# Kernel tuning notes

Hardware: AMD Instinct MI355X
Metric: run time of the kernel (lower is better)

The kernel has to match this reference:

```python
import jax, jax.numpy as jnp
import numpy as np

N_HEADS = 16
D_MODEL = 1024
SEQ = 1024
WIDTH = 32
BATCH = 4


def _make_graph(n, w, seed=0):
    # Mirrors sparse_attention_graph: normal offsets around each node index,
    # mod n, then per-row duplicates are replaced by global-ish tokens 0,1,...
    rng = np.random.default_rng(seed)
    pulls = rng.normal(0.0, float(w), size=(n, w)).astype(np.int64)
    adj = (pulls + np.arange(n)[:, None]) % n
    rows = []
    for r in adj:
        u = np.unique(r)
        i = 0
        while u.shape[0] < w:
            d = w - u.shape[0]
            u = np.unique(np.concatenate([np.arange(i, i + d), u]))
            i += d
        rows.append(np.sort(u))
    return jnp.asarray(np.stack(rows), dtype=jnp.int32)


def setup_inputs() -> dict:
    key = jax.random.key(0)
    ks = jax.random.split(key, 5)
    scale = 1.0 / np.sqrt(D_MODEL).astype(np.float32)
    return {
        "hidden_states": jax.random.normal(ks[0], (BATCH, SEQ, D_MODEL), jnp.float32),
        "wq_kernel": jax.random.normal(ks[1], (D_MODEL, D_MODEL), jnp.float32) * scale,
        "wq_bias": jnp.zeros((D_MODEL,), jnp.float32),
        "wk_kernel": jax.random.normal(ks[2], (D_MODEL, D_MODEL), jnp.float32) * scale,
        "wk_bias": jnp.zeros((D_MODEL,), jnp.float32),
        "wv_kernel": jax.random.normal(ks[3], (D_MODEL, D_MODEL), jnp.float32) * scale,
        "wv_bias": jnp.zeros((D_MODEL,), jnp.float32),
        "wo_kernel": jax.random.normal(ks[4], (D_MODEL, D_MODEL), jnp.float32) * scale,
        "wo_bias": jnp.zeros((D_MODEL,), jnp.float32),
        "graph": _make_graph(SEQ, WIDTH),
    }


def reference(hidden_states, wq_kernel, wq_bias, wk_kernel, wk_bias,
              wv_kernel, wv_bias, wo_kernel, wo_bias, graph):
    B, N, D = hidden_states.shape
    H = N_HEADS
    depth = D // H

    def split_heads(x):
        return x.reshape(B, N, H, depth).transpose(0, 2, 1, 3)  # [B,H,N,depth]

    q = split_heads(hidden_states @ wq_kernel + wq_bias)
    k = split_heads(hidden_states @ wk_kernel + wk_bias)
    v = split_heads(hidden_states @ wv_kernel + wv_bias)

    # Gather neighbor keys per node: [B,H,N,W,depth]; dot only on graph edges.
    kg = k[:, :, graph, :]
    dots = jnp.einsum('bhnd,bhnwd->bhnw', q, kg)

    # Scatter edge dots into dense [B,H,N,N] score matrix; non-edges stay 0,
    # exactly as dot_circle_product does (softmax then runs over the FULL row).
    rows = jnp.arange(N)[:, None]  # broadcasts with graph [N,W]
    scores = jnp.zeros((B, H, N, N), hidden_states.dtype).at[:, :, rows, graph].set(dots)

    attn = jax.nn.softmax(scores / jnp.sqrt(jnp.asarray(depth, scores.dtype)), axis=-1)
    out = jnp.einsum('bhij,bhjd->bhid', attn, v)          # [B,H,N,depth]
    out = out.transpose(0, 2, 1, 3).reshape(B, N, D)      # merge heads
    output = out @ wo_kernel + wo_bias
    return (output, attn)
```

## Files before the change

kernel.cpp:

```cpp
#include <hip/hip_runtime.h>
#include <hip/hip_bf16.h>

constexpr int B = 4;
constexpr int N = 1024;
constexpr int D = 1024;
constexpr int H = 16;
constexpr int DEPTH = 64;
constexpr int W = 32;
constexpr int LDQKV = 3072;
constexpr int SROWS = 8704;

typedef _Float16 f16x8 __attribute__((ext_vector_type(8)));
typedef float f32x4 __attribute__((ext_vector_type(4)));
typedef unsigned short us8 __attribute__((ext_vector_type(8)));
typedef unsigned short us4 __attribute__((ext_vector_type(4)));

__device__ __forceinline__ float h2f(unsigned short u) {
  return (float)__builtin_bit_cast(_Float16, u);
}

__device__ __forceinline__ void load_lds16(const void* g, void* l) {
  unsigned int lo = (unsigned int)(unsigned long long)l;
  __builtin_amdgcn_global_load_lds(
      (const __attribute__((address_space(1))) unsigned int*)g,
      (__attribute__((address_space(3))) unsigned int*)lo, 16, 0, 0);
}

__device__ __forceinline__ void fill_row(float* rowf, const float* pbuf,
                                         const float* basebuf,
                                         const int* graph, float* attn,
                                         int row, int t) {
  const int n = row & (N - 1);
  const float base = basebuf[row];
  f32x4* rw = (f32x4*)rowf;
  rw[t] = (f32x4){base, base, base, base};
  __syncthreads();
  if (t < W) rowf[graph[n * W + t]] = pbuf[(size_t)row * W + t];
  __syncthreads();
  __builtin_nontemporal_store(rw[t], (f32x4*)(attn + (size_t)row * N) + t);
}

__global__ __launch_bounds__(256) void prep_all(
    const float* __restrict__ hidden, const float* __restrict__ wq,
    const float* __restrict__ wk, const float* __restrict__ wv,
    const float* __restrict__ wo, const float* __restrict__ bq,
    const float* __restrict__ bk, const float* __restrict__ bv,
    unsigned short* __restrict__ A16, unsigned short* __restrict__ BTh,
    unsigned short* __restrict__ WoTh, float* __restrict__ biasq) {
  __shared__ float sf[64][65];
  const int t = threadIdx.x;
  int blk = blockIdx.x;

  if (blk < 2048) {
    const size_t i = ((size_t)blk * 256 + t) * 8;
    float4 a = *(const float4*)(hidden + i);
    float4 b = *(const float4*)(hidden + i + 4);
    float xs[8] = {a.x, a.y, a.z, a.w, b.x, b.y, b.z, b.w};
    us8 hv;
#pragma unroll
    for (int j = 0; j < 8; j++)
      hv[j] = __builtin_bit_cast(unsigned short, (_Float16)xs[j]);
    *(us8*)(A16 + i) = hv;
    return;
  }
  blk -= 2048;
  if (blk < 1024) {
    const int which = blk >> 8;
    const int sub = blk & 255;
    const float* w = which == 0 ? wq : which == 1 ? wk : which == 2 ? wv : wo;
    unsigned short* oh = which < 3 ? BTh : WoTh;
    const int rowOff = which < 3 ? which * 1024 : 0;

    const int tn = (sub & 15) * 64;
    const int tk = (sub >> 4) * 64;
#pragma unroll
    for (int i = 0; i < 4; i++) {
      int f = i * 256 + t;
      int r = f >> 4, c4 = (f & 15) * 4;
      float4 v = *(const float4*)(w + (size_t)(tk + r) * 1024 + tn + c4);
      sf[r][c4 + 0] = v.x; sf[r][c4 + 1] = v.y;
      sf[r][c4 + 2] = v.z; sf[r][c4 + 3] = v.w;
    }
    __syncthreads();
    const int n = t >> 2;
    const int kc = (t & 3) * 16;
    us8 hv[2];
#pragma unroll
    for (int half = 0; half < 2; half++) {
#pragma unroll
      for (int j = 0; j < 8; j++) {
        float x = sf[kc + half * 8 + j][n];
        hv[half][j] = __builtin_bit_cast(unsigned short, (_Float16)x);
      }
    }
    size_t dst = (size_t)(rowOff + tn + n) * 1024 + tk + kc;
    *(us8*)(oh + dst) = hv[0];
    *(us8*)(oh + dst + 8) = hv[1];
    return;
  }
  blk -= 1024;
  int i = blk * 256 + t;
  biasq[i] = i < 1024 ? bq[i] : (i < 2048 ? bk[i - 1024] : bv[i - 2048]);
}

__global__ __launch_bounds__(256, 2) void gemm_qkv(
    const unsigned short* __restrict__ A16, const unsigned short* __restrict__ BTh,
    const float* __restrict__ bias, unsigned short* __restrict__ Cout,
    float* __restrict__ vpart, int K, int Nn) {
  __shared__ __align__(16) unsigned short sA[2 * 128 * 32];
  __shared__ __align__(16) unsigned short sB[2 * 256 * 32];
  __shared__ float vred[2][2][8][16];

  const int tid = threadIdx.x;
  const int lane = tid & 63;
  const int wave = tid >> 6;
  const int wr = wave >> 1, wc = wave & 1;

  const int gx = gridDim.x;
  const int nwg = gx * gridDim.y;
  int bid = blockIdx.y * gx + blockIdx.x;
  bid = (bid & 7) * (nwg >> 3) + (bid >> 3);
  const int bm = (bid / gx) * 128;
  const int bn = (bid % gx) * 256;

  size_t aoff[2];
  int ldsA[2];
#pragma unroll
  for (int c = 0; c < 2; c++) {
    const int chunk = wave + 4 * c;
    const int e = chunk * 512 + lane * 8;
    const int r = e >> 5;
    const int kpos = (e >> 3) & 3;
    const int ksrc = kpos ^ ((r >> 1) & 3);
    aoff[c] = (size_t)(bm + r) * K + ksrc * 8;
    ldsA[c] = chunk * 512;
  }
  size_t boff[4];
  int ldsB[4];
#pragma unroll
  for (int c = 0; c < 4; c++) {
    const int chunk = wave + 4 * c;
    const int e = chunk * 512 + lane * 8;
    const int r = e >> 5;
    const int kpos = (e >> 3) & 3;
    const int ksrc = kpos ^ ((r >> 1) & 3);
    boff[c] = (size_t)(bn + r) * K + ksrc * 8;
    ldsB[c] = chunk * 512;
  }

  const int fr = lane & 15;
  const int fkg = lane >> 4;

  int aroff[4], broff[8];
#pragma unroll
  for (int m = 0; m < 4; m++) {
    const int ra = wr * 64 + m * 16 + fr;
    aroff[m] = ra * 32 + ((fkg ^ ((ra >> 1) & 3)) << 3);
  }
#pragma unroll
  for (int n = 0; n < 8; n++) {
    const int rb = wc * 128 + n * 16 + fr;
    broff[n] = rb * 32 + ((fkg ^ ((rb >> 1) & 3)) << 3);
  }

  f32x4 acc[4][8] = {};

  const int NT = K >> 5;
#pragma unroll
  for (int c = 0; c < 2; c++) load_lds16(A16 + aoff[c], sA + ldsA[c]);
#pragma unroll
  for (int c = 0; c < 4; c++) load_lds16(BTh + boff[c], sB + ldsB[c]);
  __syncthreads();

  int cur = 0;
  for (int t = 0; t < NT; t++) {
    const int boA = cur * (128 * 32);
    const int boB = cur * (256 * 32);
    const int nxA = (cur ^ 1) * (128 * 32);
    const int nxB = (cur ^ 1) * (256 * 32);
    if (t + 1 < NT) {
      const int k0 = (t + 1) << 5;
#pragma unroll
      for (int c = 0; c < 2; c++) load_lds16(A16 + aoff[c] + k0, sA + nxA + ldsA[c]);
#pragma unroll
      for (int c = 0; c < 4; c++) load_lds16(BTh + boff[c] + k0, sB + nxB + ldsB[c]);
    }
    f16x8 a[4], bh[8];
#pragma unroll
    for (int m = 0; m < 4; m++) a[m] = *(const f16x8*)(sA + boA + aroff[m]);
#pragma unroll
    for (int n = 0; n < 8; n++) bh[n] = *(const f16x8*)(sB + boB + broff[n]);
    __builtin_amdgcn_s_setprio(1);
#pragma unroll
    for (int m = 0; m < 4; m++)
#pragma unroll
      for (int n = 0; n < 8; n++)
        acc[m][n] = __builtin_amdgcn_mfma_f32_16x16x32_f16(a[m], bh[n], acc[m][n], 0, 0, 0);
    __builtin_amdgcn_s_setprio(0);
    __syncthreads();
    cur ^= 1;
  }

#pragma unroll
  for (int m = 0; m < 4; m++) {
    const int row = bm + wr * 64 + m * 16 + fkg * 4;
#pragma unroll
    for (int n = 0; n < 8; n++) {
      const int col = bn + wc * 128 + n * 16 + fr;
      const float bsv = bias[col];
#pragma unroll
      for (int j = 0; j < 4; j++) {
        const float v = acc[m][n][j] + bsv;
        Cout[(size_t)(row + j) * Nn + col] =
            __builtin_bit_cast(unsigned short, (_Float16)v);
      }
    }
  }

  if (bn >= 2048) {
    float csum[8];
#pragma unroll
    for (int n = 0; n < 8; n++) {
      float s = 0.f;
#pragma unroll
      for (int m = 0; m < 4; m++)
#pragma unroll
        for (int j = 0; j < 4; j++) s += acc[m][n][j];
      s += __shfl_xor(s, 16);
      s += __shfl_xor(s, 32);
      csum[n] = s;
    }
    if (fkg == 0) {
#pragma unroll
      for (int n = 0; n < 8; n++) vred[wr][wc][n][fr] = csum[n];
    }
    __syncthreads();
    if (wr == 0 && fkg == 0) {
#pragma unroll
      for (int n = 0; n < 8; n++) {
        const int d = bn - 2048 + wc * 128 + n * 16 + fr;
        vpart[(size_t)(bm >> 7) * 1024 + d] = csum[n] + vred[1][wc][n][fr];
      }
    }
  }
}

__global__ __launch_bounds__(256) void vsum_comb(const float* __restrict__ vpart,
                                                 const float* __restrict__ biasq,
                                                 float* __restrict__ vsum) {
  const int i = blockIdx.x * 256 + threadIdx.x;
  const int b = i >> 10, d = i & 1023;
  float s = 1024.0f * biasq[2048 + d];
#pragma unroll
  for (int c = 0; c < 8; c++) s += vpart[(size_t)(b * 8 + c) * 1024 + d];
  vsum[i] = s;
}

__global__ __launch_bounds__(256) void attn_pass1(
    const unsigned short* __restrict__ qkv16, const float* __restrict__ vsum,
    const int* __restrict__ graph, float* __restrict__ pbuf,
    float* __restrict__ basebuf, unsigned short* __restrict__ O16,
    float* __restrict__ attn) {
  const int blk = blockIdx.x;
  const int n = blk & (N - 1);
  const int hg = (blk >> 10) & 3;
  const int b = blk >> 12;
  const int wave = threadIdx.x >> 6;
  const int lane = threadIdx.x & 63;
  const int h = hg * 4 + wave;
  const int bid = (b * H + h) * N + n;

  __shared__ float q_sh[4][DEPTH];
  __shared__ int g_sh[W];
  __shared__ float p_sh[4][W];
  __shared__ float rowbuf[4][N];

  const unsigned short* qrow = qkv16 + (size_t)(b * N + n) * LDQKV + h * DEPTH;
  q_sh[wave][lane] = h2f(qrow[lane]);
  if (threadIdx.x < W) g_sh[threadIdx.x] = graph[n * W + threadIdx.x];
  __syncthreads();

  const int w = lane >> 1;
  const int half = lane & 1;
  const unsigned short* krow =
      qkv16 + 1024 + (size_t)(b * N + g_sh[w]) * LDQKV + h * DEPTH + half * 32;
  float acc = 0.f;
#pragma unroll
  for (int j8 = 0; j8 < 4; j8++) {
    us8 kv = *(const us8*)(krow + j8 * 8);
    const float* qh = &q_sh[wave][half * 32 + j8 * 8];
#pragma unroll
    for (int e = 0; e < 8; e++) acc += h2f(kv[e]) * qh[e];
  }
  acc += __shfl_xor(acc, 1);
  const float dot = acc * 0.125f;

  float m = dot;
#pragma unroll
  for (int off = 2; off < 64; off <<= 1) m = fmaxf(m, __shfl_xor(m, off));
  m = fmaxf(m, 0.f);

  const float e = expf(dot - m);
  float s = e;
#pragma unroll
  for (int off = 1; off < 64; off <<= 1) s += __shfl_xor(s, off);
  s *= 0.5f;

  const float em = expf(-m);
  const float Z = (float)(N - W) * em + s;
  const float inv = 1.f / Z;
  const float base = em * inv;
  const float pw = e * inv;

  if (half == 0) p_sh[wave][w] = pw;
  __syncthreads();

  const bool fused = (bid >= SROWS);
  if (!fused) {
    if (half == 0) pbuf[(size_t)bid * W + w] = pw;
    if (lane == 0) basebuf[bid] = base;
  }

  const unsigned short* vbase = qkv16 + 2048;
  const int col = h * DEPTH + lane;
  float ov = base * vsum[b * D + col];
#pragma unroll 4
  for (int ww = 0; ww < W; ww++) {
    ov += (p_sh[wave][ww] - base) *
          h2f(vbase[(size_t)(b * N + g_sh[ww]) * LDQKV + col]);
  }
  _Float16 hh = (_Float16)ov;
  O16[(size_t)(b * N + n) * D + col] = __builtin_bit_cast(unsigned short, hh);

  f32x4* rw = (f32x4*)rowbuf[wave];
  f32x4 b4v = {base, base, base, base};
#pragma unroll
  for (int i = 0; i < 4; i++) rw[lane + 64 * i] = b4v;
  __syncthreads();
  if (fused && half == 0) rowbuf[wave][g_sh[w]] = pw;
  __syncthreads();
  if (fused) {
    f32x4* dst = (f32x4*)(attn + (size_t)bid * N);
#pragma unroll
    for (int i = 0; i < 4; i++)
      __builtin_nontemporal_store(rw[lane + 64 * i], dst + lane + 64 * i);
  }
}

__global__ __launch_bounds__(256, 4) void gemm_o_fill(
    const unsigned short* __restrict__ A16, const unsigned short* __restrict__ BTh,
    const float* __restrict__ bias, float* __restrict__ Cout,
    const float* __restrict__ pbuf, const float* __restrict__ basebuf,
    const int* __restrict__ graph, float* __restrict__ attn, int K, int Nn) {
  __shared__ __align__(16) unsigned short sA[2 * 128 * 32];
  __shared__ __align__(16) unsigned short sB[2 * 128 * 32];

  const int blk = blockIdx.x;
  if (blk >= 256) {
    fill_row((float*)sA, pbuf, basebuf, graph, attn, blk - 256, threadIdx.x);
    return;
  }

  const int tid = threadIdx.x;
  const int lane = tid & 63;
  const int wave = tid >> 6;
  const int wr = wave >> 1, wc = wave & 1;

  int bid = blk;
  bid = (bid & 7) * 32 + (bid >> 3);
  const int bm = (bid >> 3) * 128;
  const int bn = (bid & 7) * 128;

  size_t aoff[2], boff[2];
  int ldsoff[2];
#pragma unroll
  for (int c = 0; c < 2; c++) {
    const int chunk = wave + 4 * c;
    const int e = chunk * 512 + lane * 8;
    const int r = e >> 5;
    const int kpos = (e >> 3) & 3;
    const int ksrc = kpos ^ ((r >> 1) & 3);
    aoff[c] = (size_t)(bm + r) * K + ksrc * 8;
    boff[c] = (size_t)(bn + r) * K + ksrc * 8;
    ldsoff[c] = chunk * 512;
  }

  const int fr = lane & 15;
  const int fkg = lane >> 4;

  int aroff[4], broff[4];
#pragma unroll
  for (int m = 0; m < 4; m++) {
    const int ra = wr * 64 + m * 16 + fr;
    aroff[m] = ra * 32 + ((fkg ^ ((ra >> 1) & 3)) << 3);
    const int rb = wc * 64 + m * 16 + fr;
    broff[m] = rb * 32 + ((fkg ^ ((rb >> 1) & 3)) << 3);
  }

  f32x4 acc[4][4] = {};

  const int NT = K >> 5;
#pragma unroll
  for (int c = 0; c < 2; c++) {
    load_lds16(A16 + aoff[c], sA + ldsoff[c]);
    load_lds16(BTh + boff[c], sB + ldsoff[c]);
  }
  __syncthreads();

  int cur = 0;
  for (int t = 0; t < NT; t++) {
    const int bo_ = cur * (128 * 32);
    const int nx_ = (cur ^ 1) * (128 * 32);
    if (t + 1 < NT) {
      const int k0 = (t + 1) << 5;
#pragma unroll
      for (int c = 0; c < 2; c++) {
        load_lds16(A16 + aoff[c] + k0, sA + nx_ + ldsoff[c]);
        load_lds16(BTh + boff[c] + k0, sB + nx_ + ldsoff[c]);
      }
    }
    f16x8 a[4], bh[4];
#pragma unroll
    for (int m = 0; m < 4; m++) a[m] = *(const f16x8*)(sA + bo_ + aroff[m]);
#pragma unroll
    for (int n = 0; n < 4; n++) bh[n] = *(const f16x8*)(sB + bo_ + broff[n]);
    __builtin_amdgcn_s_setprio(1);
#pragma unroll
    for (int m = 0; m < 4; m++)
#pragma unroll
      for (int n = 0; n < 4; n++)
        acc[m][n] = __builtin_amdgcn_mfma_f32_16x16x32_f16(a[m], bh[n], acc[m][n], 0, 0, 0);
    __builtin_amdgcn_s_setprio(0);
    __syncthreads();
    cur ^= 1;
  }

#pragma unroll
  for (int m = 0; m < 4; m++) {
    const int row = bm + wr * 64 + m * 16 + fkg * 4;
#pragma unroll
    for (int n = 0; n < 4; n++) {
      const int col = bn + wc * 64 + n * 16 + fr;
      const float bsv = bias[col];
#pragma unroll
      for (int j = 0; j < 4; j++)
        Cout[(size_t)(row + j) * Nn + col] = acc[m][n][j] + bsv;
    }
  }
}

__global__ __launch_bounds__(256) void attn_fill_last(
    const float* __restrict__ pbuf, const float* __restrict__ basebuf,
    const int* __restrict__ graph, float* __restrict__ attn) {
  __shared__ __align__(16) float rowf[N];
  fill_row(rowf, pbuf, basebuf, graph, attn, 6144 + blockIdx.x, threadIdx.x);
}

extern "C" void kernel_launch(void* const* d_in, const int* in_sizes, int n_in,
                              void* d_out, int out_size, void* d_ws, size_t ws_size,
                              hipStream_t stream) {
  const float* hidden = (const float*)d_in[0];
  const float* wq = (const float*)d_in[1];
  const float* bq = (const float*)d_in[2];
  const float* wk = (const float*)d_in[3];
  const float* bk = (const float*)d_in[4];
  const float* wv = (const float*)d_in[5];
  const float* bv = (const float*)d_in[6];
  const float* wo = (const float*)d_in[7];
  const float* bo = (const float*)d_in[8];
  const int* graph = (const int*)d_in[9];

  float* out0 = (float*)d_out;
  float* attnp = out0 + (size_t)B * N * D;

  const size_t M1 = (size_t)1024 * 1024;
  unsigned short* qkv16 = (unsigned short*)attnp;
  unsigned short* A16 = (unsigned short*)(attnp + 6 * M1);
  unsigned short* O16 = A16;
  unsigned short* WoTh = (unsigned short*)(attnp + 8 * M1);
  unsigned short* BTh = (unsigned short*)(attnp + 8 * M1 + 524288);

  float* pbuf = (float*)d_ws;
  float* basebuf = pbuf + (size_t)B * H * N * W;
  float* vsumb = basebuf + (size_t)B * H * N;
  float* biasq = pbuf;
  float* vpart = pbuf + 4096;

  prep_all<<<3084, 256, 0, stream>>>(hidden, wq, wk, wv, wo, bq, bk, bv,
                                     A16, BTh, WoTh, biasq);

  gemm_qkv<<<dim3(12, 32), 256, 0, stream>>>(A16, BTh, biasq, qkv16, vpart,
                                             1024, 3072);

  vsum_comb<<<16, 256, 0, stream>>>(vpart, biasq, vsumb);

  attn_pass1<<<B * 4 * N, 256, 0, stream>>>(qkv16, vsumb, graph, pbuf, basebuf,
                                            O16, attnp);

  gemm_o_fill<<<256 + 6144, 256, 0, stream>>>(O16, WoTh, bo, out0, pbuf,
                                              basebuf, graph, attnp,
                                              1024, 1024);

  attn_fill_last<<<8704 - 6144, 256, 0, stream>>>(pbuf, basebuf, graph, attnp);
}
```

Measured before the change: 146.2 us.

## Fuse hidden-state fp16 conversion into QKV GEMM and drop vsum kernel

The QKV GEMM now loads fp32 hidden states straight into LDS with a new swizzle and converts them to fp16 on the fly. This removes the separate conversion pass in prep_all and its A16 buffer round trip. The vsum_comb kernel is also removed, and each attn_pass1 thread now sums the 8 V-column partials itself, which drops one launch but repeats that small reduction in every block. The cost is twice the LDS traffic for A and extra conversion instructions inside the GEMM main loop. The reduction scratch space now reuses sA after a barrier.

New measurement: 148.3 us. About the same (+1.5%).

```diff
diff --git a/kernel.cpp b/kernel.cpp
--- a/kernel.cpp
+++ b/kernel.cpp
@@ -41,29 +41,15 @@
 }
 
 __global__ __launch_bounds__(256) void prep_all(
-    const float* __restrict__ hidden, const float* __restrict__ wq,
-    const float* __restrict__ wk, const float* __restrict__ wv,
-    const float* __restrict__ wo, const float* __restrict__ bq,
-    const float* __restrict__ bk, const float* __restrict__ bv,
-    unsigned short* __restrict__ A16, unsigned short* __restrict__ BTh,
+    const float* __restrict__ wq, const float* __restrict__ wk,
+    const float* __restrict__ wv, const float* __restrict__ wo,
+    const float* __restrict__ bq, const float* __restrict__ bk,
+    const float* __restrict__ bv, unsigned short* __restrict__ BTh,
     unsigned short* __restrict__ WoTh, float* __restrict__ biasq) {
   __shared__ float sf[64][65];
   const int t = threadIdx.x;
   int blk = blockIdx.x;
 
-  if (blk < 2048) {
-    const size_t i = ((size_t)blk * 256 + t) * 8;
-    float4 a = *(const float4*)(hidden + i);
-    float4 b = *(const float4*)(hidden + i + 4);
-    float xs[8] = {a.x, a.y, a.z, a.w, b.x, b.y, b.z, b.w};
-    us8 hv;
-#pragma unroll
-    for (int j = 0; j < 8; j++)
-      hv[j] = __builtin_bit_cast(unsigned short, (_Float16)xs[j]);
-    *(us8*)(A16 + i) = hv;
-    return;
-  }
-  blk -= 2048;
   if (blk < 1024) {
     const int which = blk >> 8;
     const int sub = blk & 255;
@@ -104,12 +90,11 @@
 }
 
 __global__ __launch_bounds__(256, 2) void gemm_qkv(
-    const unsigned short* __restrict__ A16, const unsigned short* __restrict__ BTh,
+    const float* __restrict__ hidden, const unsigned short* __restrict__ BTh,
     const float* __restrict__ bias, unsigned short* __restrict__ Cout,
     float* __restrict__ vpart, int K, int Nn) {
-  __shared__ __align__(16) unsigned short sA[2 * 128 * 32];
+  __shared__ __align__(16) float sA[2 * 128 * 32];
   __shared__ __align__(16) unsigned short sB[2 * 256 * 32];
-  __shared__ float vred[2][2][8][16];
 
   const int tid = threadIdx.x;
   const int lane = tid & 63;
@@ -123,17 +108,17 @@
   const int bm = (bid / gx) * 128;
   const int bn = (bid % gx) * 256;
 
-  size_t aoff[2];
-  int ldsA[2];
-#pragma unroll
-  for (int c = 0; c < 2; c++) {
+  size_t aoff[4];
+  int ldsA[4];
+#pragma unroll
+  for (int c = 0; c < 4; c++) {
     const int chunk = wave + 4 * c;
-    const int e = chunk * 512 + lane * 8;
+    const int e = chunk * 256 + lane * 4;
     const int r = e >> 5;
-    const int kpos = (e >> 3) & 3;
-    const int ksrc = kpos ^ ((r >> 1) & 3);
-    aoff[c] = (size_t)(bm + r) * K + ksrc * 8;
-    ldsA[c] = chunk * 512;
+    const int g = (e >> 2) & 7;
+    const int gs = g ^ (r & 7);
+    aoff[c] = (size_t)(bm + r) * K + gs * 4;
+    ldsA[c] = chunk * 256;
   }
   size_t boff[4];
   int ldsB[4];
@@ -151,12 +136,16 @@
   const int fr = lane & 15;
   const int fkg = lane >> 4;
 
-  int aroff[4], broff[8];
+  int ar0[4], ar1[4];
 #pragma unroll
   for (int m = 0; m < 4; m++) {
     const int ra = wr * 64 + m * 16 + fr;
-    aroff[m] = ra * 32 + ((fkg ^ ((ra >> 1) & 3)) << 3);
-  }
+    const int s = ra & 7;
+    const int g0 = (2 * fkg) ^ s;
+    ar0[m] = ra * 32 + g0 * 4;
+    ar1[m] = ra * 32 + (g0 ^ 1) * 4;
+  }
+  int broff[8];
 #pragma unroll
   for (int n = 0; n < 8; n++) {
     const int rb = wc * 128 + n * 16 + fr;
@@ -167,9 +156,10 @@
 
   const int NT = K >> 5;
 #pragma unroll
-  for (int c = 0; c < 2; c++) load_lds16(A16 + aoff[c], sA + ldsA[c]);
-#pragma unroll
-  for (int c = 0; c < 4; c++) load_lds16(BTh + boff[c], sB + ldsB[c]);
+  for (int c = 0; c < 4; c++) {
+    load_lds16(hidden + aoff[c], sA + ldsA[c]);
+    load_lds16(BTh + boff[c], sB + ldsB[c]);
+  }
   __syncthreads();
 
   int cur = 0;
@@ -181,13 +171,22 @@
     if (t + 1 < NT) {
       const int k0 = (t + 1) << 5;
 #pragma unroll
-      for (int c = 0; c < 2; c++) load_lds16(A16 + aoff[c] + k0, sA + nxA + ldsA[c]);
-#pragma unroll
-      for (int c = 0; c < 4; c++) load_lds16(BTh + boff[c] + k0, sB + nxB + ldsB[c]);
+      for (int c = 0; c < 4; c++) {
+        load_lds16(hidden + aoff[c] + k0, sA + nxA + ldsA[c]);
+        load_lds16(BTh + boff[c] + k0, sB + nxB + ldsB[c]);
+      }
     }
     f16x8 a[4], bh[8];
 #pragma unroll
-    for (int m = 0; m < 4; m++) a[m] = *(const f16x8*)(sA + boA + aroff[m]);
+    for (int m = 0; m < 4; m++) {
+      f32x4 lo = *(const f32x4*)(sA + boA + ar0[m]);
+      f32x4 hi = *(const f32x4*)(sA + boA + ar1[m]);
+#pragma unroll
+      for (int j = 0; j < 4; j++) {
+        a[m][j] = (_Float16)lo[j];
+        a[m][j + 4] = (_Float16)hi[j];
+      }
+    }
 #pragma unroll
     for (int n = 0; n < 8; n++) bh[n] = *(const f16x8*)(sB + boB + broff[n]);
     __builtin_amdgcn_s_setprio(1);
@@ -218,6 +217,7 @@
   }
 
   if (bn >= 2048) {
+    float* vred = (float*)sA;
     float csum[8];
 #pragma unroll
     for (int n = 0; n < 8; n++) {
@@ -230,37 +230,29 @@
       s += __shfl_xor(s, 32);
       csum[n] = s;
     }
+    __syncthreads();
     if (fkg == 0) {
 #pragma unroll
-      for (int n = 0; n < 8; n++) vred[wr][wc][n][fr] = csum[n];
+      for (int n = 0; n < 8; n++)
+        vred[(((wr * 2 + wc) * 8) + n) * 16 + fr] = csum[n];
     }
     __syncthreads();
     if (wr == 0 && fkg == 0) {
 #pragma unroll
       for (int n = 0; n < 8; n++) {
         const int d = bn - 2048 + wc * 128 + n * 16 + fr;
-        vpart[(size_t)(bm >> 7) * 1024 + d] = csum[n] + vred[1][wc][n][fr];
-      }
-    }
-  }
-}
-
-__global__ __launch_bounds__(256) void vsum_comb(const float* __restrict__ vpart,
-                                                 const float* __restrict__ biasq,
-                                                 float* __restrict__ vsum) {
-  const int i = blockIdx.x * 256 + threadIdx.x;
-  const int b = i >> 10, d = i & 1023;
-  float s = 1024.0f * biasq[2048 + d];
-#pragma unroll
-  for (int c = 0; c < 8; c++) s += vpart[(size_t)(b * 8 + c) * 1024 + d];
-  vsum[i] = s;
+        vpart[(size_t)(bm >> 7) * 1024 + d] =
+            csum[n] + vred[(((1 * 2 + wc) * 8) + n) * 16 + fr];
+      }
+    }
+  }
 }
 
 __global__ __launch_bounds__(256) void attn_pass1(
-    const unsigned short* __restrict__ qkv16, const float* __restrict__ vsum,
-    const int* __restrict__ graph, float* __restrict__ pbuf,
-    float* __restrict__ basebuf, unsigned short* __restrict__ O16,
-    float* __restrict__ attn) {
+    const unsigned short* __restrict__ qkv16, const float* __restrict__ vpart,
+    const float* __restrict__ biasq, const int* __restrict__ graph,
+    float* __restrict__ pbuf, float* __restrict__ basebuf,
+    unsigned short* __restrict__ O16, float* __restrict__ attn) {
   const int blk = blockIdx.x;
   const int n = blk & (N - 1);
   const int hg = (blk >> 10) & 3;
@@ -321,9 +313,13 @@
     if (lane == 0) basebuf[bid] = base;
   }
 
+  const int col = h * DEPTH + lane;
+  float vs = 1024.0f * biasq[2048 + col];
+#pragma unroll
+  for (int c = 0; c < 8; c++) vs += vpart[(size_t)(b * 8 + c) * 1024 + col];
+
   const unsigned short* vbase = qkv16 + 2048;
-  const int col = h * DEPTH + lane;
-  float ov = base * vsum[b * D + col];
+  float ov = base * vs;
 #pragma unroll 4
   for (int ww = 0; ww < W; ww++) {
     ov += (p_sh[wave][ww] - base) *
@@ -475,27 +471,23 @@
 
   const size_t M1 = (size_t)1024 * 1024;
   unsigned short* qkv16 = (unsigned short*)attnp;
-  unsigned short* A16 = (unsigned short*)(attnp + 6 * M1);
-  unsigned short* O16 = A16;
+  unsigned short* O16 = (unsigned short*)(attnp + 6 * M1);
   unsigned short* WoTh = (unsigned short*)(attnp + 8 * M1);
   unsigned short* BTh = (unsigned short*)(attnp + 8 * M1 + 524288);
 
   float* pbuf = (float*)d_ws;
   float* basebuf = pbuf + (size_t)B * H * N * W;
-  float* vsumb = basebuf + (size_t)B * H * N;
-  float* biasq = pbuf;
-  float* vpart = pbuf + 4096;
-
-  prep_all<<<3084, 256, 0, stream>>>(hidden, wq, wk, wv, wo, bq, bk, bv,
-                                     A16, BTh, WoTh, biasq);
-
-  gemm_qkv<<<dim3(12, 32), 256, 0, stream>>>(A16, BTh, biasq, qkv16, vpart,
+  float* biasq = basebuf + (size_t)B * H * N;
+  float* vpart = biasq + 4096;
+
+  prep_all<<<1036, 256, 0, stream>>>(wq, wk, wv, wo, bq, bk, bv,
+                                     BTh, WoTh, biasq);
+
+  gemm_qkv<<<dim3(12, 32), 256, 0, stream>>>(hidden, BTh, biasq, qkv16, vpart,
                                              1024, 3072);
 
-  vsum_comb<<<16, 256, 0, stream>>>(vpart, biasq, vsumb);
-
-  attn_pass1<<<B * 4 * N, 256, 0, stream>>>(qkv16, vsumb, graph, pbuf, basebuf,
-                                            O16, attnp);
+  attn_pass1<<<B * 4 * N, 256, 0, stream>>>(qkv16, vpart, biasq, graph, pbuf,
+                                            basebuf, O16, attnp);
 
   gemm_o_fill<<<256 + 6144, 256, 0, stream>>>(O16, WoTh, bo, out0, pbuf,
                                               basebuf, graph, attnp,
```

## Fold vsum reduction into attn_pass1 and relocate buffers to workspace when large

Applied to the files above, without the earlier changes.

Drops the separate vsum_comb kernel; each attn_pass1 thread now sums the eight V column partials plus the scaled bias itself. When the workspace is large enough, O16 and the transposed Wo weights move out of the attn output region into workspace. More attn rows can then be written directly in pass1 (srows 6144), and the trailing attn_fill_last launch is skipped. The trade-offs are redundant vpart reads across the 1024 row blocks and a dependence on the harness-provided workspace size.

After: 137.9 us (median of 2 runs). -5.7%, faster.

```diff
diff --git a/kernel.cpp b/kernel.cpp
--- a/kernel.cpp
+++ b/kernel.cpp
@@ -8,7 +8,6 @@
 constexpr int DEPTH = 64;
 constexpr int W = 32;
 constexpr int LDQKV = 3072;
-constexpr int SROWS = 8704;
 
 typedef _Float16 f16x8 __attribute__((ext_vector_type(8)));
 typedef float f32x4 __attribute__((ext_vector_type(4)));
@@ -245,22 +244,11 @@
   }
 }
 
-__global__ __launch_bounds__(256) void vsum_comb(const float* __restrict__ vpart,
-                                                 const float* __restrict__ biasq,
-                                                 float* __restrict__ vsum) {
-  const int i = blockIdx.x * 256 + threadIdx.x;
-  const int b = i >> 10, d = i & 1023;
-  float s = 1024.0f * biasq[2048 + d];
-#pragma unroll
-  for (int c = 0; c < 8; c++) s += vpart[(size_t)(b * 8 + c) * 1024 + d];
-  vsum[i] = s;
-}
-
 __global__ __launch_bounds__(256) void attn_pass1(
-    const unsigned short* __restrict__ qkv16, const float* __restrict__ vsum,
-    const int* __restrict__ graph, float* __restrict__ pbuf,
-    float* __restrict__ basebuf, unsigned short* __restrict__ O16,
-    float* __restrict__ attn) {
+    const unsigned short* __restrict__ qkv16, const float* __restrict__ vpart,
+    const float* __restrict__ biasq, const int* __restrict__ graph,
+    float* __restrict__ pbuf, float* __restrict__ basebuf,
+    unsigned short* __restrict__ O16, float* __restrict__ attn, int srows) {
   const int blk = blockIdx.x;
   const int n = blk & (N - 1);
   const int hg = (blk >> 10) & 3;
@@ -315,15 +303,19 @@
   if (half == 0) p_sh[wave][w] = pw;
   __syncthreads();
 
-  const bool fused = (bid >= SROWS);
+  const bool fused = (bid >= srows);
   if (!fused) {
     if (half == 0) pbuf[(size_t)bid * W + w] = pw;
     if (lane == 0) basebuf[bid] = base;
   }
 
+  const int col = h * DEPTH + lane;
+  float vs = 1024.0f * biasq[2048 + col];
+#pragma unroll
+  for (int c = 0; c < 8; c++) vs += vpart[(size_t)(b * 8 + c) * 1024 + col];
+
   const unsigned short* vbase = qkv16 + 2048;
-  const int col = h * DEPTH + lane;
-  float ov = base * vsum[b * D + col];
+  float ov = base * vs;
 #pragma unroll 4
   for (int ww = 0; ww < W; ww++) {
     ov += (p_sh[wave][ww] - base) *
@@ -474,17 +466,33 @@
   float* attnp = out0 + (size_t)B * N * D;
 
   const size_t M1 = (size_t)1024 * 1024;
+
+  float* pbuf = (float*)d_ws;
+  float* basebuf = pbuf + (size_t)B * H * N * W;
+  float* biasq = basebuf + (size_t)B * H * N;
+  float* vpart = biasq + 4096;
+  float* ws_end = vpart + 32768;
+
   unsigned short* qkv16 = (unsigned short*)attnp;
   unsigned short* A16 = (unsigned short*)(attnp + 6 * M1);
-  unsigned short* O16 = A16;
-  unsigned short* WoTh = (unsigned short*)(attnp + 8 * M1);
-  unsigned short* BTh = (unsigned short*)(attnp + 8 * M1 + 524288);
-
-  float* pbuf = (float*)d_ws;
-  float* basebuf = pbuf + (size_t)B * H * N * W;
-  float* vsumb = basebuf + (size_t)B * H * N;
-  float* biasq = pbuf;
-  float* vpart = pbuf + 4096;
+
+  const size_t need = ((size_t)ws_end - (size_t)d_ws) +
+                      (4 * M1 + 1 * M1) * sizeof(unsigned short);
+  const bool bigws = ws_size >= need;
+
+  unsigned short *O16, *WoTh, *BTh;
+  int srows;
+  if (bigws) {
+    O16 = (unsigned short*)ws_end;
+    WoTh = O16 + 4 * M1;
+    BTh = (unsigned short*)(attnp + 8 * M1);
+    srows = 6144;
+  } else {
+    O16 = A16;
+    WoTh = (unsigned short*)(attnp + 8 * M1);
+    BTh = (unsigned short*)(attnp + 8 * M1 + 524288);
+    srows = 8704;
+  }
 
   prep_all<<<3084, 256, 0, stream>>>(hidden, wq, wk, wv, wo, bq, bk, bv,
                                      A16, BTh, WoTh, biasq);
@@ -492,14 +500,14 @@
   gemm_qkv<<<dim3(12, 32), 256, 0, stream>>>(A16, BTh, biasq, qkv16, vpart,
                                              1024, 3072);
 
-  vsum_comb<<<16, 256, 0, stream>>>(vpart, biasq, vsumb);
-
-  attn_pass1<<<B * 4 * N, 256, 0, stream>>>(qkv16, vsumb, graph, pbuf, basebuf,
-                                            O16, attnp);
+  attn_pass1<<<B * 4 * N, 256, 0, stream>>>(qkv16, vpart, biasq, graph, pbuf,
+                                            basebuf, O16, attnp, srows);
 
   gemm_o_fill<<<256 + 6144, 256, 0, stream>>>(O16, WoTh, bo, out0, pbuf,
                                               basebuf, graph, attnp,
                                               1024, 1024);
 
-  attn_fill_last<<<8704 - 6144, 256, 0, stream>>>(pbuf, basebuf, graph, attnp);
-}
+  if (srows > 6144)
+    attn_fill_last<<<srows - 6144, 256, 0, stream>>>(pbuf, basebuf, graph,
+                                                     attnp);
+}
```
